# Optimization experiments

Hardware: AMD Instinct MI355X
Metric: run time of the kernel (lower is better)

The kernel has to match this reference:

```python
import jax, jax.numpy as jnp
import numpy as np

B, P, ENC = 128, 196, 2048   # batch, num_pixels (14x14), encoder_dim
A, H, E, V = 512, 512, 512, 10000  # attention_dim, hidden, embed, vocab
T = 20  # max decode length (lengths max = T+1)


def setup_inputs() -> dict:
    key = jax.random.key(0)
    ks = jax.random.split(key, 24)
    def rn(k, shape, scale=0.05):
        return jax.random.normal(k, shape, jnp.float32) * scale
    encoder_out = jax.random.normal(ks[0], (B, P, ENC), jnp.float32)
    captions = jax.random.randint(ks[1], (B, T + 1), 0, V)
    # lengths sorted descending (packed-sequence convention), max forced to T+1
    lengths = jnp.sort(jax.random.randint(ks[2], (B,), 2, T + 2))[::-1]
    lengths = lengths.at[0].set(T + 1)
    return {
        "encoder_out": encoder_out,
        "captions": captions,
        "lengths": lengths,
        "W_enc_att": rn(ks[3], (A, ENC)), "b_enc_att": jnp.zeros((A,), jnp.float32),
        "W_dec_att": rn(ks[4], (A, H)),   "b_dec_att": jnp.zeros((A,), jnp.float32),
        "w_full_att": rn(ks[5], (1, A)),  "b_full_att": jnp.zeros((1,), jnp.float32),
        "emb_table": rn(ks[6], (V, E)),
        "W_ih": rn(ks[7], (4 * H, E + ENC)), "b_ih": jnp.zeros((4 * H,), jnp.float32),
        "W_hh": rn(ks[8], (4 * H, H)),       "b_hh": jnp.zeros((4 * H,), jnp.float32),
        "W_init_h": rn(ks[9], (H, ENC)),  "b_init_h": jnp.zeros((H,), jnp.float32),
        "W_init_c": rn(ks[10], (H, ENC)), "b_init_c": jnp.zeros((H,), jnp.float32),
        "W_fbeta": rn(ks[11], (ENC, H)),  "b_fbeta": jnp.zeros((ENC,), jnp.float32),
        "W_fc": rn(ks[12], (V, H)),       "b_fc": jnp.zeros((V,), jnp.float32),
    }


def reference(encoder_out, captions, lengths,
              W_enc_att, b_enc_att, W_dec_att, b_dec_att, w_full_att, b_full_att,
              emb_table, W_ih, b_ih, W_hh, b_hh,
              W_init_h, b_init_h, W_init_c, b_init_c,
              W_fbeta, b_fbeta, W_fc, b_fc):
    # Precompute encoder side of Bahdanau attention once (loop-invariant)
    att1 = jnp.einsum('bpe,ae->bpa', encoder_out, W_enc_att) + b_enc_att  # [B,P,A]
    emb = emb_table[captions]                                            # [B,T+1,E]
    mean_enc = encoder_out.mean(axis=1)                                  # [B,ENC]
    h0 = mean_enc @ W_init_h.T + b_init_h
    c0 = mean_enc @ W_init_c.T + b_init_c
    dec_len = lengths - 1
    # mask[t, b] = True while sample b still decodes at step t (== torch's b < batch_size_t for sorted lengths)
    mask = (jnp.arange(T)[:, None] < dec_len[None, :]).astype(encoder_out.dtype)  # [T,B]
    xs = (jnp.swapaxes(emb[:, :T, :], 0, 1), mask)  # ([T,B,E], [T,B])

    def step(carry, x):
        h, c = carry
        emb_t, m = x  # [B,E], [B]
        # Bahdanau attention
        att2 = h @ W_dec_att.T + b_dec_att                               # [B,A]
        e = jnp.einsum('bpa,a->bp', jax.nn.relu(att1 + att2[:, None, :]),
                       w_full_att[0]) + b_full_att[0]                    # [B,P]
        alpha = jax.nn.softmax(e, axis=1)
        context = jnp.einsum('bp,bpe->be', alpha, encoder_out)           # [B,ENC]
        gate = jax.nn.sigmoid(h @ W_fbeta.T + b_fbeta)
        context = gate * context
        # LSTMCell (PyTorch gate order: i, f, g, o); dropout is identity in eval mode
        x_in = jnp.concatenate([emb_t, context], axis=1)                 # [B,E+ENC]
        gates = x_in @ W_ih.T + b_ih + h @ W_hh.T + b_hh                 # [B,4H]
        i, f, g, o = jnp.split(gates, 4, axis=1)
        c_new = jax.nn.sigmoid(f) * c + jax.nn.sigmoid(i) * jnp.tanh(g)
        h_new = jax.nn.sigmoid(o) * jnp.tanh(c_new)
        pred = (h_new @ W_fc.T + b_fc) * m[:, None]                      # zeros past length
        mb = m[:, None]
        h = mb * h_new + (1.0 - mb) * h   # freeze state for finished rows
        c = mb * c_new + (1.0 - mb) * c
        return (h, c), pred

    (_, _), preds = jax.lax.scan(step, (h0, c0), xs)
    return jnp.swapaxes(preds, 0, 1)  # [B,T,V]
```

## Files before the change

### kernel.cpp

```cpp
#include <hip/hip_runtime.h>
#include <hip/hip_bf16.h>
#include <math.h>

#define B_   128
#define P_   196
#define ENC_ 2048
#define A_   512
#define H_   512
#define E_   512
#define V_   10000
#define T_   20
#define NDF_ 2560
#define XK_  3072
#define GK_  2560

typedef __attribute__((ext_vector_type(8))) short bf16x8;
typedef __attribute__((ext_vector_type(4))) short bf16x4;
typedef __attribute__((ext_vector_type(2))) short bf16x2;
typedef __attribute__((ext_vector_type(4))) float f32x4;

__device__ __forceinline__ float sigmoidf_(float x) { return 1.0f / (1.0f + expf(-x)); }

__device__ __forceinline__ short f2bf(float f) {
    unsigned u = __float_as_uint(f);
    u += 0x7fffu + ((u >> 16) & 1u);
    return (short)(u >> 16);
}
__device__ __forceinline__ float bf2f(short s) {
    return __uint_as_float(((unsigned)(unsigned short)s) << 16);
}
__device__ __forceinline__ void gload_lds16(const void* g, void* l) {
    __builtin_amdgcn_global_load_lds(
        (const __attribute__((address_space(1))) void*)g,
        (__attribute__((address_space(3))) void*)l, 16, 0, 0);
}

#define BM 128
#define BN 64
#define BK 64

#define COMPUTE64(ASP, BSP, CUR)                                               \
    _Pragma("unroll")                                                          \
    for (int kk = 0; kk < BK; kk += 32) {                                      \
        const int kb = (kk >> 3) + (lane >> 4);                                \
        bf16x8 av[4], bv[2];                                                   \
        _Pragma("unroll")                                                      \
        for (int i = 0; i < 4; i++) {                                          \
            int rr = wr * 64 + i * 16 + (lane & 15);                           \
            av[i] = *(const bf16x8*)&(ASP)[(CUR) * (BM * BK) + rr * BK         \
                    + ((kb ^ (rr & 7)) << 3)];                                 \
        }                                                                      \
        _Pragma("unroll")                                                      \
        for (int j = 0; j < 2; j++) {                                          \
            int cc = wc * 32 + j * 16 + (lane & 15);                           \
            bv[j] = *(const bf16x8*)&(BSP)[(CUR) * (BN * BK) + cc * BK         \
                    + ((kb ^ (cc & 7)) << 3)];                                 \
        }                                                                      \
        _Pragma("unroll")                                                      \
        for (int i = 0; i < 4; i++)                                            \
            _Pragma("unroll")                                                  \
            for (int j = 0; j < 2; j++)                                        \
                acc[i][j] = __builtin_amdgcn_mfma_f32_16x16x32_bf16(           \
                    av[i], bv[j], acc[i][j], 0, 0, 0);                         \
    }

__global__ __launch_bounds__(256) void gemm_bf(
    const short* __restrict__ A, const short* __restrict__ Bw,
    float* __restrict__ Cf, short* __restrict__ Cb,
    const float* __restrict__ bias,
    int N, int K, int lda, int ldb, int ldc,
    int mtiles, int ntiles, int mode,
    const int* __restrict__ lengths)
{
    __shared__ __attribute__((aligned(16))) short As[2][BM * BK];
    __shared__ __attribute__((aligned(16))) short Bs[2][BN * BK];
    int pm, pn;
    if (mtiles == 1) { pm = 0; pn = blockIdx.x; }
    else {
        int xcd = blockIdx.x & 7, s = blockIdx.x >> 3;
        pn = s % ntiles;
        pm = (s / ntiles) * 8 + xcd;
        if (pm >= mtiles) return;
    }
    const int bm = pm * BM, bn = pn * BN;
    const int tid = threadIdx.x, w = tid >> 6, lane = tid & 63;
    const int wr = w >> 1, wc = w & 1;
    const int lr8 = lane >> 3, lk = lane & 7;

    f32x4 zero4 = {0.f, 0.f, 0.f, 0.f};
    f32x4 acc[4][2];
    #pragma unroll
    for (int i = 0; i < 4; i++)
        #pragma unroll
        for (int j = 0; j < 2; j++) acc[i][j] = zero4;

#define STAGE(buf, k0) {                                                        \
    _Pragma("unroll")                                                           \
    for (int i = 0; i < 4; i++) {                                               \
        int row0 = w * 32 + i * 8; int row = row0 + lr8;                        \
        gload_lds16(A + (size_t)(bm + row) * lda + (k0)                         \
                    + ((lk ^ (row & 7)) << 3), &As[buf][row0 * BK]);            \
    }                                                                           \
    _Pragma("unroll")                                                           \
    for (int i = 0; i < 2; i++) {                                               \
        int row0 = w * 16 + i * 8; int row = row0 + lr8;                        \
        int gn = bn + row; if (gn > N - 1) gn = N - 1;                          \
        gload_lds16(Bw + (size_t)gn * ldb + (k0)                                \
                    + ((lk ^ (row & 7)) << 3), &Bs[buf][row0 * BK]);            \
    } }

    STAGE(0, 0);
    __syncthreads();
    int cur = 0;
    for (int k0 = 0; k0 < K; k0 += BK) {
        if (k0 + BK < K) STAGE(cur ^ 1, k0 + BK);
        COMPUTE64(&As[0][0], &Bs[0][0], cur);
        __syncthreads();
        cur ^= 1;
    }
#undef STAGE

    const int lr = lane >> 4, lc = lane & 15;
    #pragma unroll
    for (int i = 0; i < 4; i++) {
        #pragma unroll
        for (int r = 0; r < 4; r++) {
            int row = bm + wr * 64 + i * 16 + lr * 4 + r;
            #pragma unroll
            for (int j = 0; j < 2; j++) {
                int col = bn + wc * 32 + j * 16 + lc;
                if (col >= N) continue;
                float v = acc[i][j][r] + bias[col];
                if (mode == 1) {
                    int tt = row >> 7, bb = row & 127;
                    float rs = (tt < lengths[bb] - 1) ? 1.0f : 0.0f;
                    Cf[(size_t)bb * T_ * V_ + (size_t)tt * V_ + col] = v * rs;
                } else if (mode == 2) {
                    if (col < H_) Cb[(size_t)row * H_ + col] = f2bf(v);
                    else          Cf[(size_t)row * H_ + (col - H_)] = v;
                } else if (Cb) {
                    Cb[(size_t)row * ldc + col] = f2bf(v);
                } else {
                    Cf[(size_t)row * ldc + col] = v;
                }
            }
        }
    }
}

__global__ __launch_bounds__(256) void gemm_bf64(
    const short* __restrict__ A, const short* __restrict__ Bw,
    short* __restrict__ Cb, const float* __restrict__ bias,
    int N, int K, int lda, int ldb, int ldc,
    int mtiles, int ntiles)
{
    __shared__ __attribute__((aligned(16))) short As[2][64 * BK];
    __shared__ __attribute__((aligned(16))) short Bs[2][BN * BK];
    int xcd = blockIdx.x & 7, s = blockIdx.x >> 3;
    int pn = s % ntiles;
    int pm = (s / ntiles) * 8 + xcd;
    if (pm >= mtiles) return;
    const int bm = pm * 64, bn = pn * BN;
    const int tid = threadIdx.x, w = tid >> 6, lane = tid & 63;
    const int wr = w >> 1, wc = w & 1;
    const int lr8 = lane >> 3, lk = lane & 7;

    f32x4 zero4 = {0.f, 0.f, 0.f, 0.f};
    f32x4 acc[2][2];
    #pragma unroll
    for (int i = 0; i < 2; i++)
        #pragma unroll
        for (int j = 0; j < 2; j++) acc[i][j] = zero4;

#define STAGE64(buf, k0) {                                                      \
    _Pragma("unroll")                                                           \
    for (int i = 0; i < 2; i++) {                                               \
        int row0 = w * 16 + i * 8; int row = row0 + lr8;                        \
        gload_lds16(A + (size_t)(bm + row) * lda + (k0)                         \
                    + ((lk ^ (row & 7)) << 3), &As[buf][row0 * BK]);            \
    }                                                                           \
    _Pragma("unroll")                                                           \
    for (int i = 0; i < 2; i++) {                                               \
        int row0 = w * 16 + i * 8; int row = row0 + lr8;                        \
        int gn = bn + row; if (gn > N - 1) gn = N - 1;                          \
        gload_lds16(Bw + (size_t)gn * ldb + (k0)                                \
                    + ((lk ^ (row & 7)) << 3), &Bs[buf][row0 * BK]);            \
    } }

    STAGE64(0, 0);
    __syncthreads();
    int cur = 0;
    for (int k0 = 0; k0 < K; k0 += BK) {
        if (k0 + BK < K) STAGE64(cur ^ 1, k0 + BK);
        #pragma unroll
        for (int kk = 0; kk < BK; kk += 32) {
            const int kb = (kk >> 3) + (lane >> 4);
            bf16x8 av[2], bv[2];
            #pragma unroll
            for (int i = 0; i < 2; i++) {
                int rr = wr * 32 + i * 16 + (lane & 15);
                av[i] = *(const bf16x8*)&As[cur][rr * BK + ((kb ^ (rr & 7)) << 3)];
            }
            #pragma unroll
            for (int j = 0; j < 2; j++) {
                int cc = wc * 32 + j * 16 + (lane & 15);
                bv[j] = *(const bf16x8*)&Bs[cur][cc * BK + ((kb ^ (cc & 7)) << 3)];
            }
            #pragma unroll
            for (int i = 0; i < 2; i++)
                #pragma unroll
                for (int j = 0; j < 2; j++)
                    acc[i][j] = __builtin_amdgcn_mfma_f32_16x16x32_bf16(
                        av[i], bv[j], acc[i][j], 0, 0, 0);
        }
        __syncthreads();
        cur ^= 1;
    }
#undef STAGE64

    const int lr = lane >> 4, lc = lane & 15;
    #pragma unroll
    for (int i = 0; i < 2; i++)
        #pragma unroll
        for (int r = 0; r < 4; r++) {
            int row = bm + wr * 32 + i * 16 + lr * 4 + r;
            #pragma unroll
            for (int j = 0; j < 2; j++) {
                int col = bn + wc * 32 + j * 16 + lc;
                if (col < N) Cb[(size_t)row * ldc + col] = f2bf(acc[i][j][r] + bias[col]);
            }
        }
}

__global__ __launch_bounds__(512) void esmctx_kernel(
    const short* __restrict__ att1_bf, const float* __restrict__ attf,
    const float* __restrict__ wfull, const short* __restrict__ enc_bf,
    short* __restrict__ ctxbuf, const int* __restrict__ lengths, int t)
{
    __shared__ float es[P_];
    __shared__ float red[256];
    __shared__ float al[P_];
    __shared__ float sm, ss;
    const int b = blockIdx.y, half = blockIdx.x;
    if (t >= lengths[b] - 1) return;
    const int tid = threadIdx.x, wv = tid >> 6, lane = tid & 63;

    float a2v[8], wv8[8];
    const float* a2 = attf + (size_t)b * NDF_;
    #pragma unroll
    for (int i = 0; i < 8; i++) {
        a2v[i] = a2[lane * 8 + i];
        wv8[i] = wfull[lane * 8 + i];
    }
    for (int row = wv; row < P_; row += 8) {
        bf16x8 a1 = *(const bf16x8*)(att1_bf + ((size_t)b * P_ + row) * A_ + lane * 8);
        float s = 0.0f;
        #pragma unroll
        for (int i = 0; i < 8; i++) {
            float v = bf2f(a1[i]) + a2v[i];
            s += fmaxf(v, 0.0f) * wv8[i];
        }
        #pragma unroll
        for (int off = 32; off > 0; off >>= 1) s += __shfl_down(s, off, 64);
        if (lane == 0) es[row] = s;
    }
    __syncthreads();
    float v = (tid < P_) ? es[tid] : -1e30f;
    if (tid < 256) red[tid] = v;
    __syncthreads();
    for (int rs = 128; rs > 0; rs >>= 1) {
        if (tid < rs) red[tid] = fmaxf(red[tid], red[tid + rs]);
        __syncthreads();
    }
    if (tid == 0) sm = red[0];
    __syncthreads();
    float ex = (tid < P_) ? expf(v - sm) : 0.0f;
    if (tid < 256) red[tid] = ex;
    __syncthreads();
    for (int rs = 128; rs > 0; rs >>= 1) {
        if (tid < rs) red[tid] += red[tid + rs];
        __syncthreads();
    }
    if (tid == 0) ss = red[0];
    __syncthreads();
    if (tid < P_) al[tid] = ex / ss;
    __syncthreads();

    const int c0 = half * 1024 + tid * 2;
    const short* eb = enc_bf + (size_t)b * P_ * ENC_ + c0;
    float s0 = 0, s1 = 0;
    for (int p = 0; p < P_; p++) {
        bf16x2 ev = *(const bf16x2*)(eb + (size_t)p * ENC_);
        float a = al[p];
        s0 += a * bf2f(ev[0]); s1 += a * bf2f(ev[1]);
    }
    const float* fb = attf + (size_t)b * NDF_ + A_;
    bf16x2 o;
    o[0] = f2bf(sigmoidf_(fb[c0 + 0]) * s0);
    o[1] = f2bf(sigmoidf_(fb[c0 + 1]) * s1);
    *(bf16x2*)(ctxbuf + (size_t)b * ENC_ + c0) = o;
}

__global__ __launch_bounds__(256) void gates_lstm(
    const short* __restrict__ ctxbuf, const short* __restrict__ hcur,
    short* __restrict__ hnxt,
    const short* __restrict__ Wcat, const float* __restrict__ gpre,
    float* __restrict__ cbuf, short* __restrict__ hn_t,
    const int* __restrict__ lengths, int t)
{
    __shared__ __attribute__((aligned(16))) char smem[49152];
    short* As0 = (short*)smem;
    short* Bs0 = (short*)(smem + 32768);
    const int bn = blockIdx.x * BN;
    const int tid = threadIdx.x, w = tid >> 6, lane = tid & 63;
    const int wr = w >> 1, wc = w & 1;
    const int lr8 = lane >> 3, lk = lane & 7;

    f32x4 zero4 = {0.f, 0.f, 0.f, 0.f};
    f32x4 acc[4][2];
    #pragma unroll
    for (int i = 0; i < 4; i++)
        #pragma unroll
        for (int j = 0; j < 2; j++) acc[i][j] = zero4;

#define STAGE_G(buf, k0) {                                                      \
    const short* Ap; int Al, kk0;                                               \
    if ((k0) < ENC_) { Ap = ctxbuf; Al = ENC_; kk0 = (k0); }                    \
    else             { Ap = hcur;   Al = H_;   kk0 = (k0) - ENC_; }             \
    _Pragma("unroll")                                                           \
    for (int i = 0; i < 4; i++) {                                               \
        int row0 = w * 32 + i * 8; int row = row0 + lr8;                        \
        gload_lds16(Ap + (size_t)row * Al + kk0 + ((lk ^ (row & 7)) << 3),      \
                    &As0[(buf) * (BM * BK) + row0 * BK]);                       \
    }                                                                           \
    _Pragma("unroll")                                                           \
    for (int i = 0; i < 2; i++) {                                               \
        int row0 = w * 16 + i * 8; int row = row0 + lr8;                        \
        gload_lds16(Wcat + (size_t)(bn + row) * XK_ + E_ + (k0)                 \
                    + ((lk ^ (row & 7)) << 3),                                  \
                    &Bs0[(buf) * (BN * BK) + row0 * BK]);                       \
    } }

    STAGE_G(0, 0);
    __syncthreads();
    int cur = 0;
    for (int k0 = 0; k0 < GK_; k0 += BK) {
        if (k0 + BK < GK_) STAGE_G(cur ^ 1, k0 + BK);
        COMPUTE64(As0, Bs0, cur);
        __syncthreads();
        cur ^= 1;
    }
#undef STAGE_G

    float* gl = (float*)smem;
    const int lr = lane >> 4, lc = lane & 15;
    #pragma unroll
    for (int i = 0; i < 4; i++)
        #pragma unroll
        for (int r = 0; r < 4; r++) {
            int row = wr * 64 + i * 16 + lr * 4 + r;
            #pragma unroll
            for (int j = 0; j < 2; j++) {
                int col = wc * 32 + j * 16 + lc;
                gl[row * 68 + col] = acc[i][j][r] + gpre[(size_t)row * (4 * H_) + bn + col];
            }
        }
    __syncthreads();
    #pragma unroll
    for (int q = 0; q < 8; q++) {
        int id  = tid * 8 + q;
        int row = id >> 4;
        int j   = id & 15;
        int jg  = (bn >> 2) + j;
        float i_ = sigmoidf_(gl[row * 68 + 4 * j + 0]);
        float f_ = sigmoidf_(gl[row * 68 + 4 * j + 1]);
        float g_ = tanhf    (gl[row * 68 + 4 * j + 2]);
        float o_ = sigmoidf_(gl[row * 68 + 4 * j + 3]);
        float cn = f_ * cbuf[row * H_ + jg] + i_ * g_;
        float hv = o_ * tanhf(cn);
        hn_t[row * H_ + jg] = f2bf(hv);
        bool m = t < lengths[row] - 1;
        if (m) cbuf[row * H_ + jg] = cn;
        hnxt[row * H_ + jg] = m ? f2bf(hv) : hcur[row * H_ + jg];
    }
}

__global__ __launch_bounds__(256) void castenc_mean(const float* __restrict__ enc,
                                                    short* __restrict__ enc_bf,
                                                    short* __restrict__ meanE_bf)
{
    const int b = blockIdx.y;
    const int c0 = blockIdx.x * 1024 + threadIdx.x * 4;
    const f32x4* src = (const f32x4*)(enc + (size_t)b * P_ * ENC_ + c0);
    short* dst = enc_bf + (size_t)b * P_ * ENC_ + c0;
    float s0 = 0, s1 = 0, s2 = 0, s3 = 0;
    for (int p = 0; p < P_; p++) {
        f32x4 f = __builtin_nontemporal_load(src + (size_t)p * (ENC_ / 4));
        bf16x4 v;
        v[0] = f2bf(f[0]); v[1] = f2bf(f[1]); v[2] = f2bf(f[2]); v[3] = f2bf(f[3]);
        *(bf16x4*)(dst + (size_t)p * ENC_) = v;
        s0 += f[0]; s1 += f[1]; s2 += f[2]; s3 += f[3];
    }
    const float inv = 1.0f / (float)P_;
    bf16x4 m;
    m[0] = f2bf(s0 * inv); m[1] = f2bf(s1 * inv);
    m[2] = f2bf(s2 * inv); m[3] = f2bf(s3 * inv);
    *(bf16x4*)(meanE_bf + (size_t)b * ENC_ + c0) = m;
}

#define PB0 1024
#define PB1 (PB0 + 2048)
#define PB2 (PB1 + 5000)
#define PB3 (PB2 + 1280)
#define PB4 (PB3 + 6144)
#define PB5 (PB4 + 1280)
#define PB6 (PB5 + 3)
#define PB7 (PB6 + 2)
#define PB8 (PB7 + 1)

__device__ __forceinline__ void cast4(const float* __restrict__ in,
                                      short* __restrict__ out, int i4) {
    float4 f = *(const float4*)(in + i4);
    bf16x4 v;
    v[0] = f2bf(f.x); v[1] = f2bf(f.y); v[2] = f2bf(f.z); v[3] = f2bf(f.w);
    *(bf16x4*)(out + i4) = v;
}
__device__ __forceinline__ void cast4p(const float* __restrict__ src,
                                       short* __restrict__ out, int i4) {
    float4 f = *(const float4*)src;
    bf16x4 v;
    v[0] = f2bf(f.x); v[1] = f2bf(f.y); v[2] = f2bf(f.z); v[3] = f2bf(f.w);
    *(bf16x4*)(out + i4) = v;
}

__global__ __launch_bounds__(256) void prep_kernel(
    const float* __restrict__ W_enc,    const float* __restrict__ W_init_h,
    const float* __restrict__ W_init_c, const float* __restrict__ W_fc,
    const float* __restrict__ W_dec,    const float* __restrict__ W_fbeta,
    const float* __restrict__ W_ih,     const float* __restrict__ W_hh,
    const int*   __restrict__ captions, const float* __restrict__ emb_tab,
    const float* __restrict__ b_dec,    const float* __restrict__ b_fbeta,
    const float* __restrict__ b_ih,     const float* __restrict__ b_hh,
    const float* __restrict__ b_init_h, const float* __restrict__ b_init_c,
    short* __restrict__ Wenc_bf,  short* __restrict__ Winit_bf,
    short* __restrict__ Wfc_bf,   short* __restrict__ Wdf_bf,
    short* __restrict__ Wcat_bf,  short* __restrict__ emb_all,
    float* __restrict__ bdf,      float* __restrict__ bcat,
    float* __restrict__ binit)
{
    const int blk = blockIdx.x, tid = threadIdx.x;
    if (blk < PB0) {
        cast4(W_enc, Wenc_bf, blk * 1024 + tid * 4);
    } else if (blk < PB1) {
        int i4 = (blk - PB0) * 1024 + tid * 4;
        int n = i4 >> 11, k = i4 & 2047;
        const float* src = (n < H_) ? W_init_h + (size_t)n * ENC_ + k
                                    : W_init_c + (size_t)(n - H_) * ENC_ + k;
        cast4p(src, Winit_bf, i4);
    } else if (blk < PB2) {
        cast4(W_fc, Wfc_bf, (blk - PB1) * 1024 + tid * 4);
    } else if (blk < PB3) {
        int i4 = (blk - PB2) * 1024 + tid * 4;
        int n = i4 >> 9, k = i4 & 511;
        const float* src = (n < A_) ? W_dec + (size_t)n * H_ + k
                                    : W_fbeta + (size_t)(n - A_) * H_ + k;
        cast4p(src, Wdf_bf, i4);
    } else if (blk < PB4) {
        int i4 = (blk - PB3) * 1024 + tid * 4;
        int n = i4 / XK_, k = i4 - n * XK_;
        int srow = (n & 3) * H_ + (n >> 2);
        const float* src = (k < E_ + ENC_) ? W_ih + (size_t)srow * (E_ + ENC_) + k
                                           : W_hh + (size_t)srow * H_ + (k - (E_ + ENC_));
        cast4p(src, Wcat_bf, i4);
    } else if (blk < PB5) {
        int i4 = (blk - PB4) * 1024 + tid * 4;
        int col = i4 & 511;
        int bt  = i4 >> 9;
        int b   = bt & 127;
        int tt  = bt >> 7;
        int tok = captions[b * (T_ + 1) + tt];
        cast4p(emb_tab + (size_t)tok * E_ + col, emb_all, i4);
    } else if (blk < PB6) {
        int j = (blk - PB5) * 1024 + tid * 4;
        #pragma unroll
        for (int q = 0; q < 4; q++, j++)
            if (j < NDF_) bdf[j] = (j < A_) ? b_dec[j] : b_fbeta[j - A_];
    } else if (blk < PB7) {
        int j = (blk - PB6) * 1024 + tid * 4;
        #pragma unroll
        for (int q = 0; q < 4; q++, j++) {
            int srow = (j & 3) * H_ + (j >> 2);
            bcat[j] = b_ih[srow] + b_hh[srow];
        }
    } else {
        int j = tid * 4;
        #pragma unroll
        for (int q = 0; q < 4; q++, j++)
            binit[j] = (j < H_) ? b_init_h[j] : b_init_c[j - H_];
    }
}

extern "C" void kernel_launch(void* const* d_in, const int* in_sizes, int n_in,
                              void* d_out, int out_size, void* d_ws, size_t ws_size,
                              hipStream_t stream)
{
    const float* enc      = (const float*)d_in[0];
    const int*   captions = (const int*)  d_in[1];
    const int*   lengths  = (const int*)  d_in[2];
    const float* W_enc    = (const float*)d_in[3];
    const float* b_enc    = (const float*)d_in[4];
    const float* W_dec    = (const float*)d_in[5];
    const float* b_dec    = (const float*)d_in[6];
    const float* w_full   = (const float*)d_in[7];
    const float* emb_tab  = (const float*)d_in[9];
    const float* W_ih     = (const float*)d_in[10];
    const float* b_ih     = (const float*)d_in[11];
    const float* W_hh     = (const float*)d_in[12];
    const float* b_hh     = (const float*)d_in[13];
    const float* W_init_h = (const float*)d_in[14];
    const float* b_init_h = (const float*)d_in[15];
    const float* W_init_c = (const float*)d_in[16];
    const float* b_init_c = (const float*)d_in[17];
    const float* W_fbeta  = (const float*)d_in[18];
    const float* b_fbeta  = (const float*)d_in[19];
    const float* W_fc     = (const float*)d_in[20];
    const float* b_fc     = (const float*)d_in[21];
    float* out = (float*)d_out;

    char* ws = (char*)d_ws;
    size_t off = 0;
    auto alloc = [&](size_t bytes) { void* p = ws + off; off += (bytes + 255) & ~(size_t)255; return p; };
    short* enc_bf    = (short*)alloc((size_t)B_ * P_ * ENC_ * 2);
    short* att1_bf   = (short*)alloc((size_t)B_ * P_ * A_ * 2);
    short* Wenc_bf   = (short*)alloc((size_t)A_ * ENC_ * 2);
    short* Winit_bf  = (short*)alloc((size_t)2 * H_ * ENC_ * 2);
    short* Wdf_bf    = (short*)alloc((size_t)NDF_ * H_ * 2);
    short* Wcat_bf   = (short*)alloc((size_t)4 * H_ * XK_ * 2);
    short* Wfc_bf    = (short*)alloc((size_t)V_ * H_ * 2);
    float* bdf       = (float*)alloc(NDF_ * 4);
    float* bcat      = (float*)alloc(4 * H_ * 4);
    float* binit     = (float*)alloc(2 * H_ * 4);
    short* meanE_bf  = (short*)alloc((size_t)B_ * ENC_ * 2);
    float* cbuf      = (float*)alloc((size_t)B_ * H_ * 4);
    short* hbufs     = (short*)alloc((size_t)2 * B_ * H_ * 2);
    short* emb_all   = (short*)alloc((size_t)T_ * B_ * E_ * 2);
    short* hn_all    = (short*)alloc((size_t)T_ * B_ * H_ * 2);
    float* attf      = (float*)alloc((size_t)B_ * NDF_ * 4);
    short* ctxbuf    = (short*)alloc((size_t)B_ * ENC_ * 2);
    float* gates_pre = (float*)alloc((size_t)T_ * B_ * 4 * H_ * 4);
    (void)ws_size;

    prep_kernel<<<PB8, 256, 0, stream>>>(
        W_enc, W_init_h, W_init_c, W_fc, W_dec, W_fbeta, W_ih, W_hh,
        captions, emb_tab, b_dec, b_fbeta, b_ih, b_hh, b_init_h, b_init_c,
        Wenc_bf, Winit_bf, Wfc_bf, Wdf_bf, Wcat_bf, emb_all, bdf, bcat, binit);
    castenc_mean<<<dim3(2, B_), 256, 0, stream>>>(enc, enc_bf, meanE_bf);
    gemm_bf64<<<8 * 8 * ((392 + 7) / 8), 256, 0, stream>>>(
        enc_bf, Wenc_bf, att1_bf, b_enc,
        A_, ENC_, ENC_, ENC_, A_, 392, 8);
    gemm_bf<<<8 * 32 * (((T_ * B_) / BM + 7) / 8), 256, 0, stream>>>(
        emb_all, Wcat_bf, gates_pre, nullptr, bcat,
        4 * H_, E_, E_, XK_, 4 * H_, (T_ * B_) / BM, 32, 0, nullptr);
    gemm_bf<<<(2 * H_) / BN, 256, 0, stream>>>(
        meanE_bf, Winit_bf, cbuf, hbufs, binit,
        2 * H_, ENC_, ENC_, ENC_, 0, 1, (2 * H_) / BN, 2, nullptr);

    for (int t = 0; t < T_; t++) {
        short* hcur = hbufs + (size_t)(t & 1) * B_ * H_;
        short* hnxt = hbufs + (size_t)((t & 1) ^ 1) * B_ * H_;
        gemm_bf<<<NDF_ / BN, 256, 0, stream>>>(
            hcur, Wdf_bf, attf, nullptr, bdf,
            NDF_, H_, H_, H_, NDF_, 1, NDF_ / BN, 0, nullptr);
        esmctx_kernel<<<dim3(2, B_), 512, 0, stream>>>(
            att1_bf, attf, w_full, enc_bf, ctxbuf, lengths, t);
        gates_lstm<<<(4 * H_) / BN, 256, 0, stream>>>(
            ctxbuf, hcur, hnxt, Wcat_bf, gates_pre + (size_t)t * B_ * 4 * H_,
            cbuf, hn_all + (size_t)t * B_ * H_, lengths, t);
    }
    gemm_bf<<<8 * 157 * (((T_ * B_) / BM + 7) / 8), 256, 0, stream>>>(
        hn_all, Wfc_bf, out, nullptr, b_fc,
        V_, H_, H_, H_, 0, (T_ * B_) / BM, 157, 1, lengths);
}
```

Measured before the change: 1.820 ms.

## Split recurrent GEMMs into 64-row tiles to raise block count per step

The per-step decoder-attention GEMM now uses the 64x64 bf16 kernel and writes a bf16 output instead of fp32. The esmctx kernel reads that bf16 buffer and converts it on load. The LSTM gates kernel is rewritten with 64-row M tiles, so it launches 64 blocks instead of 32, each with a smaller accumulator and shared-memory footprint. The goal is to fill more of the GPU's compute units in the small, latency-bound recurrent loop and to halve attention-projection traffic. The cost is extra bf16 rounding of the attention and gate pre-activations, and more blocks reloading the same weight columns.

```diff
diff --git a/kernel.cpp b/kernel.cpp
--- a/kernel.cpp
+++ b/kernel.cpp
@@ -233,7 +233,7 @@
 }
 
 __global__ __launch_bounds__(512) void esmctx_kernel(
-    const short* __restrict__ att1_bf, const float* __restrict__ attf,
+    const short* __restrict__ att1_bf, const short* __restrict__ attf_bf,
     const float* __restrict__ wfull, const short* __restrict__ enc_bf,
     short* __restrict__ ctxbuf, const int* __restrict__ lengths, int t)
 {
@@ -246,11 +246,13 @@
     const int tid = threadIdx.x, wv = tid >> 6, lane = tid & 63;
 
     float a2v[8], wv8[8];
-    const float* a2 = attf + (size_t)b * NDF_;
-    #pragma unroll
-    for (int i = 0; i < 8; i++) {
-        a2v[i] = a2[lane * 8 + i];
-        wv8[i] = wfull[lane * 8 + i];
+    {
+        bf16x8 a2x = *(const bf16x8*)(attf_bf + (size_t)b * NDF_ + lane * 8);
+        #pragma unroll
+        for (int i = 0; i < 8; i++) {
+            a2v[i] = bf2f(a2x[i]);
+            wv8[i] = wfull[lane * 8 + i];
+        }
     }
     for (int row = wv; row < P_; row += 8) {
         bf16x8 a1 = *(const bf16x8*)(att1_bf + ((size_t)b * P_ + row) * A_ + lane * 8);
@@ -294,94 +296,118 @@
         float a = al[p];
         s0 += a * bf2f(ev[0]); s1 += a * bf2f(ev[1]);
     }
-    const float* fb = attf + (size_t)b * NDF_ + A_;
+    const short* fb = attf_bf + (size_t)b * NDF_ + A_;
     bf16x2 o;
-    o[0] = f2bf(sigmoidf_(fb[c0 + 0]) * s0);
-    o[1] = f2bf(sigmoidf_(fb[c0 + 1]) * s1);
+    o[0] = f2bf(sigmoidf_(bf2f(fb[c0 + 0])) * s0);
+    o[1] = f2bf(sigmoidf_(bf2f(fb[c0 + 1])) * s1);
     *(bf16x2*)(ctxbuf + (size_t)b * ENC_ + c0) = o;
 }
 
-__global__ __launch_bounds__(256) void gates_lstm(
+__global__ __launch_bounds__(256) void gates_lstm64(
     const short* __restrict__ ctxbuf, const short* __restrict__ hcur,
     short* __restrict__ hnxt,
     const short* __restrict__ Wcat, const float* __restrict__ gpre,
     float* __restrict__ cbuf, short* __restrict__ hn_t,
     const int* __restrict__ lengths, int t)
 {
-    __shared__ __attribute__((aligned(16))) char smem[49152];
+    __shared__ __attribute__((aligned(16))) char smem[32768];
     short* As0 = (short*)smem;
-    short* Bs0 = (short*)(smem + 32768);
-    const int bn = blockIdx.x * BN;
+    short* Bs0 = (short*)(smem + 16384);
+    const int pm = blockIdx.x & 1, pn = blockIdx.x >> 1;
+    const int bm = pm * 64, bn = pn * BN;
     const int tid = threadIdx.x, w = tid >> 6, lane = tid & 63;
     const int wr = w >> 1, wc = w & 1;
     const int lr8 = lane >> 3, lk = lane & 7;
 
     f32x4 zero4 = {0.f, 0.f, 0.f, 0.f};
-    f32x4 acc[4][2];
+    f32x4 acc[2][2];
     #pragma unroll
-    for (int i = 0; i < 4; i++)
+    for (int i = 0; i < 2; i++)
         #pragma unroll
         for (int j = 0; j < 2; j++) acc[i][j] = zero4;
 
-#define STAGE_G(buf, k0) {                                                      \
+#define STAGE_G64(buf, k0) {                                                    \
     const short* Ap; int Al, kk0;                                               \
     if ((k0) < ENC_) { Ap = ctxbuf; Al = ENC_; kk0 = (k0); }                    \
     else             { Ap = hcur;   Al = H_;   kk0 = (k0) - ENC_; }             \
     _Pragma("unroll")                                                           \
-    for (int i = 0; i < 4; i++) {                                               \
-        int row0 = w * 32 + i * 8; int row = row0 + lr8;                        \
-        gload_lds16(Ap + (size_t)row * Al + kk0 + ((lk ^ (row & 7)) << 3),      \
-                    &As0[(buf) * (BM * BK) + row0 * BK]);                       \
+    for (int i = 0; i < 2; i++) {                                               \
+        int row0 = w * 16 + i * 8; int row = row0 + lr8;                        \
+        gload_lds16(Ap + (size_t)(bm + row) * Al + kk0                          \
+                    + ((lk ^ (row & 7)) << 3),                                  \
+                    &As0[(buf) * 4096 + row0 * BK]);                            \
     }                                                                           \
     _Pragma("unroll")                                                           \
     for (int i = 0; i < 2; i++) {                                               \
         int row0 = w * 16 + i * 8; int row = row0 + lr8;                        \
         gload_lds16(Wcat + (size_t)(bn + row) * XK_ + E_ + (k0)                 \
                     + ((lk ^ (row & 7)) << 3),                                  \
-                    &Bs0[(buf) * (BN * BK) + row0 * BK]);                       \
+                    &Bs0[(buf) * 4096 + row0 * BK]);                            \
     } }
 
-    STAGE_G(0, 0);
+    STAGE_G64(0, 0);
     __syncthreads();
     int cur = 0;
     for (int k0 = 0; k0 < GK_; k0 += BK) {
-        if (k0 + BK < GK_) STAGE_G(cur ^ 1, k0 + BK);
-        COMPUTE64(As0, Bs0, cur);
+        if (k0 + BK < GK_) STAGE_G64(cur ^ 1, k0 + BK);
+        #pragma unroll
+        for (int kk = 0; kk < BK; kk += 32) {
+            const int kb = (kk >> 3) + (lane >> 4);
+            bf16x8 av[2], bv[2];
+            #pragma unroll
+            for (int i = 0; i < 2; i++) {
+                int rr = wr * 32 + i * 16 + (lane & 15);
+                av[i] = *(const bf16x8*)&As0[cur * 4096 + rr * BK + ((kb ^ (rr & 7)) << 3)];
+            }
+            #pragma unroll
+            for (int j = 0; j < 2; j++) {
+                int cc = wc * 32 + j * 16 + (lane & 15);
+                bv[j] = *(const bf16x8*)&Bs0[cur * 4096 + cc * BK + ((kb ^ (cc & 7)) << 3)];
+            }
+            #pragma unroll
+            for (int i = 0; i < 2; i++)
+                #pragma unroll
+                for (int j = 0; j < 2; j++)
+                    acc[i][j] = __builtin_amdgcn_mfma_f32_16x16x32_bf16(
+                        av[i], bv[j], acc[i][j], 0, 0, 0);
+        }
         __syncthreads();
         cur ^= 1;
     }
-#undef STAGE_G
+#undef STAGE_G64
 
     float* gl = (float*)smem;
     const int lr = lane >> 4, lc = lane & 15;
     #pragma unroll
-    for (int i = 0; i < 4; i++)
+    for (int i = 0; i < 2; i++)
         #pragma unroll
         for (int r = 0; r < 4; r++) {
-            int row = wr * 64 + i * 16 + lr * 4 + r;
+            int row = wr * 32 + i * 16 + lr * 4 + r;
             #pragma unroll
             for (int j = 0; j < 2; j++) {
                 int col = wc * 32 + j * 16 + lc;
-                gl[row * 68 + col] = acc[i][j][r] + gpre[(size_t)row * (4 * H_) + bn + col];
+                gl[row * 68 + col] = acc[i][j][r]
+                    + gpre[(size_t)(bm + row) * (4 * H_) + bn + col];
             }
         }
     __syncthreads();
     #pragma unroll
-    for (int q = 0; q < 8; q++) {
-        int id  = tid * 8 + q;
-        int row = id >> 4;
-        int j   = id & 15;
-        int jg  = (bn >> 2) + j;
-        float i_ = sigmoidf_(gl[row * 68 + 4 * j + 0]);
-        float f_ = sigmoidf_(gl[row * 68 + 4 * j + 1]);
-        float g_ = tanhf    (gl[row * 68 + 4 * j + 2]);
-        float o_ = sigmoidf_(gl[row * 68 + 4 * j + 3]);
-        float cn = f_ * cbuf[row * H_ + jg] + i_ * g_;
+    for (int q = 0; q < 4; q++) {
+        int id    = tid * 4 + q;
+        int row_l = id >> 4;
+        int j     = id & 15;
+        int row_g = bm + row_l;
+        int jg    = (bn >> 2) + j;
+        float i_ = sigmoidf_(gl[row_l * 68 + 4 * j + 0]);
+        float f_ = sigmoidf_(gl[row_l * 68 + 4 * j + 1]);
+        float g_ = tanhf    (gl[row_l * 68 + 4 * j + 2]);
+        float o_ = sigmoidf_(gl[row_l * 68 + 4 * j + 3]);
+        float cn = f_ * cbuf[row_g * H_ + jg] + i_ * g_;
         float hv = o_ * tanhf(cn);
-        hn_t[row * H_ + jg] = f2bf(hv);
-        bool m = t < lengths[row] - 1;
-        if (m) cbuf[row * H_ + jg] = cn;
-        hnxt[row * H_ + jg] = m ? f2bf(hv) : hcur[row * H_ + jg];
+        hn_t[row_g * H_ + jg] = f2bf(hv);
+        bool m = t < lengths[row_g] - 1;
+        if (m) cbuf[row_g * H_ + jg] = cn;
+        hnxt[row_g * H_ + jg] = m ? f2bf(hv) : hcur[row_g * H_ + jg];
     }
 }
 
@@ -545,7 +571,7 @@
     short* hbufs     = (short*)alloc((size_t)2 * B_ * H_ * 2);
     short* emb_all   = (short*)alloc((size_t)T_ * B_ * E_ * 2);
     short* hn_all    = (short*)alloc((size_t)T_ * B_ * H_ * 2);
-    float* attf      = (float*)alloc((size_t)B_ * NDF_ * 4);
+    short* attf_bf   = (short*)alloc((size_t)B_ * NDF_ * 2);
     short* ctxbuf    = (short*)alloc((size_t)B_ * ENC_ * 2);
     float* gates_pre = (float*)alloc((size_t)T_ * B_ * 4 * H_ * 4);
     (void)ws_size;
@@ -568,12 +594,12 @@
     for (int t = 0; t < T_; t++) {
         short* hcur = hbufs + (size_t)(t & 1) * B_ * H_;
         short* hnxt = hbufs + (size_t)((t & 1) ^ 1) * B_ * H_;
-        gemm_bf<<<NDF_ / BN, 256, 0, stream>>>(
-            hcur, Wdf_bf, attf, nullptr, bdf,
-            NDF_, H_, H_, H_, NDF_, 1, NDF_ / BN, 0, nullptr);
+        gemm_bf64<<<8 * 40 * 1, 256, 0, stream>>>(
+            hcur, Wdf_bf, attf_bf, bdf,
+            NDF_, H_, H_, H_, NDF_, 2, 40);
         esmctx_kernel<<<dim3(2, B_), 512, 0, stream>>>(
-            att1_bf, attf, w_full, enc_bf, ctxbuf, lengths, t);
-        gates_lstm<<<(4 * H_) / BN, 256, 0, stream>>>(
+            att1_bf, attf_bf, w_full, enc_bf, ctxbuf, lengths, t);
+        gates_lstm64<<<64, 256, 0, stream>>>(
             ctxbuf, hcur, hnxt, Wcat_bf, gates_pre + (size_t)t * B_ * 4 * H_,
             cbuf, hn_all + (size_t)t * B_ * H_, lengths, t);
     }
```

After: 1.591 ms. -12.6%, faster.
